# Optimization experiments

Hardware: AMD Instinct MI355X
Metric: run time of the kernel (lower is better)

The kernel has to match this reference:

```python
import jax, jax.numpy as jnp
import numpy as np

TW, NV, EMB, LAYERS = 25, 4, 128, 6
N, E = 65536, 262144
T_MAX = 16.0
EPS = 1e-5

def silu(x):
    return x * jax.nn.sigmoid(x)

def setup_inputs() -> dict:
    key = jax.random.key(0)
    ks = iter(jax.random.split(key, 32))
    def nrm(shape, scale=0.05):
        return jax.random.normal(next(ks), shape, jnp.float32) * scale
    inp = {}
    inp['x'] = jax.random.normal(next(ks), (N, TW), jnp.float32)
    inp['pos'] = jax.random.uniform(next(ks), (N, 1), jnp.float32)
    inp['variables'] = jax.random.uniform(next(ks), (N, NV), jnp.float32)
    inp['dt'] = jnp.full((1,), 0.1, jnp.float32)
    inp['edge_index'] = jax.random.randint(next(ks), (2, E), 0, N)
    inp['enc_W1'] = nrm((TW + NV + 1, EMB)); inp['enc_b1'] = jnp.zeros((EMB,), jnp.float32)
    inp['enc_W2'] = nrm((EMB, EMB));         inp['enc_b2'] = jnp.zeros((EMB,), jnp.float32)
    dmsg = 2 * EMB + TW + 1 + NV   # 286: x_i,x_j,u_i-u_j,pos_i-pos_j,vars_i
    dupd = 2 * EMB + NV            # 260: x, aggregated message, vars
    inp['msg_W1'] = nrm((LAYERS, dmsg, EMB)); inp['msg_b1'] = jnp.zeros((LAYERS, EMB), jnp.float32)
    inp['msg_W2'] = nrm((LAYERS, EMB, EMB));  inp['msg_b2'] = jnp.zeros((LAYERS, EMB), jnp.float32)
    inp['upd_W1'] = nrm((LAYERS, dupd, EMB)); inp['upd_b1'] = jnp.zeros((LAYERS, EMB), jnp.float32)
    inp['upd_W2'] = nrm((LAYERS, EMB, EMB));  inp['upd_b2'] = jnp.zeros((LAYERS, EMB), jnp.float32)
    inp['dec_W1'] = nrm((8, 1, 16)); inp['dec_b1'] = jnp.zeros((8,), jnp.float32)
    inp['dec_W2'] = nrm((1, 8, 14)); inp['dec_b2'] = jnp.zeros((1,), jnp.float32)
    return inp

def reference(x, pos, variables, dt, edge_index,
              enc_W1, enc_b1, enc_W2, enc_b2,
              msg_W1, msg_b1, msg_W2, msg_b2,
              upd_W1, upd_b1, upd_W2, upd_b2,
              dec_W1, dec_b1, dec_W2, dec_b2):
    vars3 = variables[:, :3]              # alpha, beta, gamma
    t = variables[:, 3:4] / T_MAX         # normalized time
    p = pos / jnp.max(pos)                # graph.pos /= pos.max()
    inp0 = jnp.concatenate([x, p, t, vars3], axis=-1)  # [N, 30]
    h = silu(silu(inp0 @ enc_W1 + enc_b1) @ enc_W2 + enc_b2)  # [N, EMB]

    src, dst = edge_index[0], edge_index[1]  # x_j = src, x_i = dst (source_to_target)
    deg = jax.ops.segment_sum(jnp.ones((E,), jnp.float32), dst, num_segments=N)
    inv_deg = (1.0 / jnp.maximum(deg, 1.0))[:, None]

    for l in range(LAYERS):
        m_in = jnp.concatenate(
            [h[dst], h[src], x[dst] - x[src], p[dst] - p[src], variables[dst]], axis=-1)
        m = silu(m_in @ msg_W1[l] + msg_b1[l])
        m = silu(m @ msg_W2[l] + msg_b2[l])                      # [E, EMB]
        agg = jax.ops.segment_sum(m, dst, num_segments=N) * inv_deg  # mean aggr
        u = silu(jnp.concatenate([h, agg, variables], axis=-1) @ upd_W1[l] + upd_b1[l])
        u = silu(u @ upd_W2[l] + upd_b2[l])
        h_new = h + u  # in_features == out_features -> residual
        # PyG InstanceNorm (affine=False), single graph (batch all zeros)
        mu = jnp.mean(h_new, axis=0, keepdims=True)
        var = jnp.var(h_new, axis=0, keepdims=True)
        h = (h_new - mu) * jax.lax.rsqrt(var + EPS)

    # decoder: Conv1d(1->8, k=16, s=3) -> SiLU -> Conv1d(8->1, k=14, s=1)
    z = h[:, None, :]  # [N, 1, EMB]
    z = jax.lax.conv_general_dilated(z, dec_W1, (3,), 'VALID',
                                     dimension_numbers=('NCH', 'OIH', 'NCH')) + dec_b1[None, :, None]
    z = silu(z)
    z = jax.lax.conv_general_dilated(z, dec_W2, (1,), 'VALID',
                                     dimension_numbers=('NCH', 'OIH', 'NCH')) + dec_b2[None, :, None]
    diff = z[:, 0, :]  # [N, TW]
    dtc = dt[0] * jnp.arange(1, TW + 1, dtype=jnp.float32)  # cumsum of dt*ones
    return jnp.tile(x[:, -1:], (1, TW)) + dtc[None, :] * diff
```

## Files before the change

### kernel.cpp

```cpp
#include <hip/hip_runtime.h>
#include <math.h>

#define N_NODES 65536
#define N_EDGES 262144
#define N_LAYERS 6
#define T_MAX_F 16.0f
#define EPS_F 1e-5f

typedef float  f32x4  __attribute__((ext_vector_type(4)));
typedef __bf16 bf16x8 __attribute__((ext_vector_type(8)));

__device__ __forceinline__ float silu_f(float v){
    return v / (1.0f + __expf(-v));
}

__device__ __forceinline__ f32x4 mfma16(bf16x8 a, bf16x8 b, f32x4 c){
    return __builtin_amdgcn_mfma_f32_16x16x32_bf16(a, b, c, 0, 0, 0);
}

#define PK_RA (6 * 20480)
#define PK_RB (6 * 20480)
#define PK_M2 (6 * 16384)
#define PK_U1 (6 * 36864)
#define PK_U2 (6 * 16384)
#define PK_TOTAL (PK_RA + PK_RB + PK_M2 + PK_U1 + PK_U2)

__global__ __launch_bounds__(256) void k_pack(const float* __restrict__ msgW1, const float* __restrict__ msgW2,
                                              const float* __restrict__ updW1, const float* __restrict__ updW2,
                                              __bf16* __restrict__ out){
    int pg = blockIdx.x * 256 + threadIdx.x;
    if (pg >= PK_TOTAL) return;
    int p = pg;
    int mode; const float* W; int perL;
    if (p < PK_RA){ mode = 0; W = msgW1; perL = 20480; }
    else if ((p -= PK_RA) < PK_RB){ mode = 1; W = msgW1; perL = 20480; }
    else if ((p -= PK_RB) < PK_M2){ mode = 2; W = msgW2; perL = 16384; }
    else if ((p -= PK_M2) < PK_U1){ mode = 3; W = updW1; perL = 36864; }
    else { p -= PK_U1; mode = 4; W = updW2; perL = 16384; }
    int l = p / perL, q = p % perL;
    int elem = q & 7, lane = (q >> 3) & 63, cb = (q >> 9) & 7, kb = q >> 12;
    int col = cb * 16 + (lane & 15);
    int k = kb * 32 + ((lane >> 4) << 3) + elem;
    float v = 0.0f;
    if (mode == 0){
        int r = -1;
        if (k < 128) r = k;
        else if (k < 153) r = 256 + (k - 128);
        else if (k == 153) r = 281;
        else if (k < 158) r = 282 + (k - 154);
        if (r >= 0) v = W[(size_t)l * 286 * 128 + (size_t)r * 128 + col];
    } else if (mode == 1){
        if (k < 128) v = W[(size_t)l * 286 * 128 + (size_t)(128 + k) * 128 + col];
        else if (k < 153) v = -W[(size_t)l * 286 * 128 + (size_t)(256 + (k - 128)) * 128 + col];
        else if (k == 153) v = -W[(size_t)l * 286 * 128 + (size_t)281 * 128 + col];
    } else {
        int Kreal = (mode == 3) ? 260 : 128;
        if (k < Kreal) v = W[(size_t)l * Kreal * 128 + (size_t)k * 128 + col];
    }
    out[pg] = (__bf16)v;
}

__global__ __launch_bounds__(256) void k_deg_max(const int* __restrict__ dst, const float* __restrict__ pos,
                                                 int* __restrict__ deg, unsigned* __restrict__ outmax){
    __shared__ float s[256];
    int tid = threadIdx.x;
    int e = blockIdx.x * 256 + tid;
    if (e < N_EDGES) atomicAdd(deg + dst[e], 1);
    if (blockIdx.x < N_NODES / 256){
        s[tid] = pos[blockIdx.x * 256 + tid];
        __syncthreads();
        for (int off = 128; off > 0; off >>= 1){
            if (tid < off) s[tid] = fmaxf(s[tid], s[tid + off]);
            __syncthreads();
        }
        if (tid == 0) atomicMax(outmax, __float_as_uint(s[0]));
    }
}

__global__ __launch_bounds__(256) void k_scan1(const int* __restrict__ deg, int* __restrict__ csum){
    __shared__ int s[256];
    int c = blockIdx.x, t = threadIdx.x;
    s[t] = deg[c * 256 + t];
    __syncthreads();
    for (int o = 128; o > 0; o >>= 1){ if (t < o) s[t] += s[t + o]; __syncthreads(); }
    if (t == 0) csum[c] = s[0];
}

__global__ __launch_bounds__(256) void k_scan2(const int* __restrict__ csum, int* __restrict__ coff){
    __shared__ int s[256];
    int t = threadIdx.x;
    s[t] = csum[t];
    __syncthreads();
    for (int o = 1; o < 256; o <<= 1){
        int v = (t >= o) ? s[t - o] : 0;
        __syncthreads();
        s[t] += v;
        __syncthreads();
    }
    coff[t] = s[t] - csum[t];
}

__global__ __launch_bounds__(256) void k_scan3(const int* __restrict__ deg, const int* __restrict__ coff,
                                               int* __restrict__ cursor){
    __shared__ int s[256];
    int c = blockIdx.x, t = threadIdx.x;
    int d = deg[c * 256 + t];
    s[t] = d;
    __syncthreads();
    for (int o = 1; o < 256; o <<= 1){
        int v = (t >= o) ? s[t - o] : 0;
        __syncthreads();
        s[t] += v;
        __syncthreads();
    }
    cursor[c * 256 + t] = coff[c] + s[t] - d;
}

__global__ __launch_bounds__(256) void k_scatter_prep(const int* __restrict__ esrc, const int* __restrict__ edst,
                                                      int* __restrict__ cursor,
                                                      int* __restrict__ ssrcS, int* __restrict__ sdstS,
                                                      const float* __restrict__ pos, const unsigned* __restrict__ maxp,
                                                      const int* __restrict__ deg,
                                                      float* __restrict__ p, float* __restrict__ invdeg){
    int e = blockIdx.x * 256 + threadIdx.x;
    if (e < N_EDGES){
        int d = edst[e];
        int slot = atomicAdd(cursor + d, 1);
        ssrcS[slot] = esrc[e];
        sdstS[slot] = d;
    }
    if (blockIdx.x < N_NODES / 256){
        int i = blockIdx.x * 256 + threadIdx.x;
        float mp = __uint_as_float(*maxp);
        p[i] = pos[i] / mp;
        invdeg[i] = 1.0f / fmaxf((float)deg[i], 1.0f);
    }
}

__device__ __forceinline__ void gemm44(const float* A, int lda, const float* W,
                                       int kq_begin, int kq_end, int r0, int c0, float acc[4][4]){
    for (int kq = kq_begin; kq < kq_end; ++kq){
        int k = kq * 4;
        float a[4][4], w[4][4];
        #pragma unroll
        for (int i = 0; i < 4; ++i){
            float4 v = *(const float4*)(A + (r0 + i) * lda + k);
            a[i][0] = v.x; a[i][1] = v.y; a[i][2] = v.z; a[i][3] = v.w;
        }
        #pragma unroll
        for (int kk = 0; kk < 4; ++kk){
            float4 v = *(const float4*)(W + (k + kk) * 128 + c0);
            w[kk][0] = v.x; w[kk][1] = v.y; w[kk][2] = v.z; w[kk][3] = v.w;
        }
        #pragma unroll
        for (int kk = 0; kk < 4; ++kk)
            #pragma unroll
            for (int i = 0; i < 4; ++i)
                #pragma unroll
                for (int j = 0; j < 4; ++j)
                    acc[i][j] = fmaf(a[i][kk], w[kk][j], acc[i][j]);
    }
}

__global__ __launch_bounds__(256) void k_enc(const float* __restrict__ x, const float* __restrict__ p,
                                             const float* __restrict__ vars,
                                             const float* __restrict__ W1, const float* __restrict__ b1,
                                             const float* __restrict__ W2, const float* __restrict__ b2,
                                             float* __restrict__ hA){
    __shared__ __align__(16) float sin_[32 * 32];
    __shared__ __align__(16) float swA[32 * 128];
    __shared__ __align__(16) float sy[32 * 128];
    int tid = threadIdx.x;
    int n0 = blockIdx.x * 32;
    for (int i = tid; i < 32 * 32; i += 256){
        int e = i >> 5, k = i & 31;
        int node = n0 + e;
        float v;
        if (k < 25)       v = x[node * 25 + k];
        else if (k == 25) v = p[node];
        else if (k == 26) v = vars[node * 4 + 3] * (1.0f / T_MAX_F);
        else if (k < 30)  v = vars[node * 4 + (k - 27)];
        else              v = 0.0f;
        sin_[e * 32 + k] = v;
    }
    for (int i = tid; i < 32 * 128; i += 256){
        int r = i >> 7;
        swA[i] = (r < 30) ? W1[i] : 0.0f;
    }
    __syncthreads();
    int c0 = (tid & 31) * 4, r0 = (tid >> 5) * 4;
    {
        float acc[4][4] = {};
        gemm44(sin_, 32, swA, 0, 8, r0, c0, acc);
        float4 bv = *(const float4*)(b1 + c0);
        float b_[4] = {bv.x, bv.y, bv.z, bv.w};
        #pragma unroll
        for (int i = 0; i < 4; ++i){
            float4 o;
            o.x = silu_f(acc[i][0] + b_[0]);
            o.y = silu_f(acc[i][1] + b_[1]);
            o.z = silu_f(acc[i][2] + b_[2]);
            o.w = silu_f(acc[i][3] + b_[3]);
            *(float4*)(sy + (r0 + i) * 128 + c0) = o;
        }
    }
    float acc2[4][4] = {};
    for (int c = 0; c < 4; ++c){
        __syncthreads();
        for (int i = tid; i < 1024; i += 256)
            ((float4*)swA)[i] = ((const float4*)(W2 + (size_t)c * 32 * 128))[i];
        __syncthreads();
        gemm44(sy + c * 32, 128, swA, 0, 8, r0, c0, acc2);
    }
    float4 b2v = *(const float4*)(b2 + c0);
    float bb[4] = {b2v.x, b2v.y, b2v.z, b2v.w};
    #pragma unroll
    for (int i = 0; i < 4; ++i){
        float4 o;
        o.x = silu_f(acc2[i][0] + bb[0]);
        o.y = silu_f(acc2[i][1] + bb[1]);
        o.z = silu_f(acc2[i][2] + bb[2]);
        o.w = silu_f(acc2[i][3] + bb[3]);
        *(float4*)(hA + (size_t)(n0 + r0 + i) * 128 + c0) = o;
    }
}

__global__ __launch_bounds__(256) void k_npre(const float* __restrict__ hA, const float* __restrict__ x,
                                              const float* __restrict__ p, const float* __restrict__ vars,
                                              const float* __restrict__ statPrev, int apply_ln,
                                              const __bf16* __restrict__ Wra, const __bf16* __restrict__ Wrb,
                                              const float* __restrict__ b1,
                                              __bf16* __restrict__ raO, __bf16* __restrict__ rbO,
                                              float* __restrict__ aggZ, float* __restrict__ statCurZ){
    __shared__ __align__(16) __bf16 sA[10 * 64 * 8];
    __shared__ __align__(16) float sOut[32 * 264];
    __shared__ __align__(16) float smu[128], sistd[128];
    int tid = threadIdx.x;
    int n0 = blockIdx.x * 32;
    if (apply_ln && tid < 128){
        float m = statPrev[tid] * (1.0f / N_NODES);
        float v = statPrev[128 + tid] * (1.0f / N_NODES) - m * m;
        smu[tid] = m;
        sistd[tid] = rsqrtf(v + EPS_F);
    }
    if (blockIdx.x == 0) statCurZ[tid] = 0.f;
    {
        float4 z4 = {0.f, 0.f, 0.f, 0.f};
        #pragma unroll
        for (int it = 0; it < 4; ++it){
            int i = tid + it * 256;
            int e = i >> 5, ch = i & 31;
            *(float4*)(aggZ + (size_t)(n0 + e) * 128 + ch * 4) = z4;
        }
    }
    __syncthreads();
    #pragma unroll
    for (int it = 0; it < 3; ++it){
        int j = tid + it * 256;
        if (j < 640){
            int f = j >> 6, lane = j & 63;
            int kb = f >> 1, mt = f & 1;
            int e = (lane & 15) + mt * 16, kh = lane >> 4;
            int node = n0 + e;
            bf16x8 o;
            if (kb < 4){
                int k0 = kb * 32 + kh * 8;
                float4 v0 = *(const float4*)(hA + (size_t)node * 128 + k0);
                float4 v1 = *(const float4*)(hA + (size_t)node * 128 + k0 + 4);
                if (apply_ln){
                    float4 m0 = *(const float4*)(smu + k0),   m1 = *(const float4*)(smu + k0 + 4);
                    float4 s0 = *(const float4*)(sistd + k0), s1 = *(const float4*)(sistd + k0 + 4);
                    v0.x = (v0.x - m0.x) * s0.x; v0.y = (v0.y - m0.y) * s0.y;
                    v0.z = (v0.z - m0.z) * s0.z; v0.w = (v0.w - m0.w) * s0.w;
                    v1.x = (v1.x - m1.x) * s1.x; v1.y = (v1.y - m1.y) * s1.y;
                    v1.z = (v1.z - m1.z) * s1.z; v1.w = (v1.w - m1.w) * s1.w;
                }
                o[0] = (__bf16)v0.x; o[1] = (__bf16)v0.y; o[2] = (__bf16)v0.z; o[3] = (__bf16)v0.w;
                o[4] = (__bf16)v1.x; o[5] = (__bf16)v1.y; o[6] = (__bf16)v1.z; o[7] = (__bf16)v1.w;
            } else {
                #pragma unroll
                for (int jj = 0; jj < 8; ++jj){
                    int fk = kh * 8 + jj;
                    float v;
                    if (fk < 25)       v = x[node * 25 + fk];
                    else if (fk == 25) v = p[node];
                    else if (fk < 30)  v = vars[node * 4 + (fk - 26)];
                    else               v = 0.0f;
                    o[jj] = (__bf16)v;
                }
            }
            *(bf16x8*)(sA + (f * 64 + lane) * 8) = o;
        }
    }
    __syncthreads();
    int w = tid >> 6, lane = tid & 63;
    int clo = lane & 15, rhi = lane >> 4;
    f32x4 z = {0.f, 0.f, 0.f, 0.f};
    f32x4 aR[2][2] = {{z, z}, {z, z}};
    f32x4 aB[2][2] = {{z, z}, {z, z}};
    #pragma unroll
    for (int kb = 0; kb < 5; ++kb){
        bf16x8 a0 = *(bf16x8*)(sA + ((kb * 2 + 0) * 64 + lane) * 8);
        bf16x8 a1 = *(bf16x8*)(sA + ((kb * 2 + 1) * 64 + lane) * 8);
        bf16x8 wr0 = *(const bf16x8*)(Wra + (size_t)((kb * 8 + 2 * w)     * 64 + lane) * 8);
        bf16x8 wr1 = *(const bf16x8*)(Wra + (size_t)((kb * 8 + 2 * w + 1) * 64 + lane) * 8);
        bf16x8 wb0 = *(const bf16x8*)(Wrb + (size_t)((kb * 8 + 2 * w)     * 64 + lane) * 8);
        bf16x8 wb1 = *(const bf16x8*)(Wrb + (size_t)((kb * 8 + 2 * w + 1) * 64 + lane) * 8);
        aR[0][0] = mfma16(a0, wr0, aR[0][0]);
        aR[0][1] = mfma16(a0, wr1, aR[0][1]);
        aR[1][0] = mfma16(a1, wr0, aR[1][0]);
        aR[1][1] = mfma16(a1, wr1, aR[1][1]);
        aB[0][0] = mfma16(a0, wb0, aB[0][0]);
        aB[0][1] = mfma16(a0, wb1, aB[0][1]);
        aB[1][0] = mfma16(a1, wb0, aB[1][0]);
        aB[1][1] = mfma16(a1, wb1, aB[1][1]);
    }
    #pragma unroll
    for (int nf = 0; nf < 2; ++nf){
        int col = (2 * w + nf) * 16 + clo;
        float bv = b1[col];
        #pragma unroll
        for (int mt = 0; mt < 2; ++mt)
            #pragma unroll
            for (int i = 0; i < 4; ++i){
                int e = mt * 16 + rhi * 4 + i;
                sOut[e * 264 + col]       = aR[mt][nf][i] + bv;
                sOut[e * 264 + 128 + col] = aB[mt][nf][i];
            }
    }
    __syncthreads();
    #pragma unroll
    for (int it = 0; it < 4; ++it){
        int j = tid + it * 256;
        int row = j >> 5, c8 = j & 31;
        const float* src = sOut + row * 264 + c8 * 8;
        bf16x8 o;
        #pragma unroll
        for (int t = 0; t < 8; ++t) o[t] = (__bf16)src[t];
        __bf16* dstp = (c8 < 16) ? (raO + (size_t)(n0 + row) * 128 + c8 * 8)
                                 : (rbO + (size_t)(n0 + row) * 128 + (c8 - 16) * 8);
        *(bf16x8*)dstp = o;
    }
}

__global__ __launch_bounds__(256) void k_edge3(const __bf16* __restrict__ ra, const __bf16* __restrict__ rb,
                                               const int* __restrict__ ssrcS, const int* __restrict__ sdstS,
                                               const __bf16* __restrict__ Wp2, const float* __restrict__ bias2,
                                               float* __restrict__ agg){
    __shared__ __align__(16) unsigned char smem[64 * 128 * 4];
    __shared__ int sd[64], ss[64];
    __bf16* sA   = (__bf16*)smem;
    float*  msum = (float*)smem;
    int tid = threadIdx.x;
    int e0 = blockIdx.x * 64;
    if (tid < 64){ sd[tid] = sdstS[e0 + tid]; ss[tid] = ssrcS[e0 + tid]; }
    __syncthreads();
    #pragma unroll
    for (int it = 0; it < 4; ++it){
        int j = tid + it * 256;
        int f = j >> 6, lane = j & 63;
        int kb = f >> 2, mt = f & 3;
        int e = (lane & 15) + mt * 16;
        int k0 = kb * 32 + (lane >> 4) * 8;
        bf16x8 va = *(const bf16x8*)(ra + (size_t)sd[e] * 128 + k0);
        bf16x8 vb = *(const bf16x8*)(rb + (size_t)ss[e] * 128 + k0);
        bf16x8 o;
        #pragma unroll
        for (int t = 0; t < 8; ++t)
            o[t] = (__bf16)silu_f((float)va[t] + (float)vb[t]);
        *(bf16x8*)(sA + (f * 64 + lane) * 8) = o;
    }
    __syncthreads();
    int w = tid >> 6, lane = tid & 63;
    int cb0 = 2 * w, clo = lane & 15, rhi = lane >> 4;
    f32x4 z = {0.f, 0.f, 0.f, 0.f};
    f32x4 acc[4][2] = {{z, z}, {z, z}, {z, z}, {z, z}};
    #pragma unroll
    for (int kb = 0; kb < 4; ++kb){
        bf16x8 a0 = *(bf16x8*)(sA + ((kb * 4 + 0) * 64 + lane) * 8);
        bf16x8 a1 = *(bf16x8*)(sA + ((kb * 4 + 1) * 64 + lane) * 8);
        bf16x8 a2 = *(bf16x8*)(sA + ((kb * 4 + 2) * 64 + lane) * 8);
        bf16x8 a3 = *(bf16x8*)(sA + ((kb * 4 + 3) * 64 + lane) * 8);
        bf16x8 w0 = *(const bf16x8*)(Wp2 + (size_t)((kb * 8 + cb0)     * 64 + lane) * 8);
        bf16x8 w1 = *(const bf16x8*)(Wp2 + (size_t)((kb * 8 + cb0 + 1) * 64 + lane) * 8);
        acc[0][0] = mfma16(a0, w0, acc[0][0]);
        acc[0][1] = mfma16(a0, w1, acc[0][1]);
        acc[1][0] = mfma16(a1, w0, acc[1][0]);
        acc[1][1] = mfma16(a1, w1, acc[1][1]);
        acc[2][0] = mfma16(a2, w0, acc[2][0]);
        acc[2][1] = mfma16(a2, w1, acc[2][1]);
        acc[3][0] = mfma16(a3, w0, acc[3][0]);
        acc[3][1] = mfma16(a3, w1, acc[3][1]);
    }
    __syncthreads();
    #pragma unroll
    for (int nf = 0; nf < 2; ++nf){
        int col = (cb0 + nf) * 16 + clo;
        float bv = bias2[col];
        #pragma unroll
        for (int mt = 0; mt < 4; ++mt)
            #pragma unroll
            for (int i = 0; i < 4; ++i){
                int row = mt * 16 + rhi * 4 + i;
                msum[row * 128 + col] = silu_f(acc[mt][nf][i] + bv);
            }
    }
    __syncthreads();
    int col = tid & 127, half = tid >> 7;
    int base = half * 32;
    float run = 0.0f;
    for (int r = 0; r < 32; ++r){
        int row = base + r;
        run += msum[row * 128 + col];
        bool flush = (r == 31) || (sd[row + 1] != sd[row]);
        if (flush){
            atomicAdd(agg + (size_t)sd[row] * 128 + col, run);
            run = 0.0f;
        }
    }
}

__global__ __launch_bounds__(256) void k_upd_m(float* __restrict__ hA, const float* __restrict__ agg,
                                               const float* __restrict__ vars, const float* __restrict__ invdeg,
                                               const float* __restrict__ statPrev, int apply_ln,
                                               const __bf16* __restrict__ Wp1, const float* __restrict__ bias1,
                                               const __bf16* __restrict__ Wp2, const float* __restrict__ bias2,
                                               float* __restrict__ statCur){
    __shared__ __align__(16) __bf16 sA1[36 * 64 * 8];
    __shared__ __align__(16) float smu[128], sistd[128];
    __bf16* zb = sA1;
    int tid = threadIdx.x;
    int n0 = blockIdx.x * 64;
    if (apply_ln && tid < 128){
        float m = statPrev[tid] * (1.0f / N_NODES);
        float v = statPrev[128 + tid] * (1.0f / N_NODES) - m * m;
        smu[tid] = m;
        sistd[tid] = rsqrtf(v + EPS_F);
    }
    __syncthreads();
    #pragma unroll
    for (int it = 0; it < 9; ++it){
        int idx = tid + it * 256;
        int f = idx >> 6, lane = idx & 63;
        int kb = f >> 2, mt = f & 3;
        int row = (lane & 15) + mt * 16;
        int node = n0 + row;
        int k0 = kb * 32 + ((lane >> 4) << 3);
        bf16x8 o;
        if (k0 < 128){
            float4 v0 = *(const float4*)(hA + (size_t)node * 128 + k0);
            float4 v1 = *(const float4*)(hA + (size_t)node * 128 + k0 + 4);
            if (apply_ln){
                float4 m0 = *(const float4*)(smu + k0),   m1 = *(const float4*)(smu + k0 + 4);
                float4 s0 = *(const float4*)(sistd + k0), s1 = *(const float4*)(sistd + k0 + 4);
                v0.x = (v0.x - m0.x) * s0.x; v0.y = (v0.y - m0.y) * s0.y;
                v0.z = (v0.z - m0.z) * s0.z; v0.w = (v0.w - m0.w) * s0.w;
                v1.x = (v1.x - m1.x) * s1.x; v1.y = (v1.y - m1.y) * s1.y;
                v1.z = (v1.z - m1.z) * s1.z; v1.w = (v1.w - m1.w) * s1.w;
            }
            o[0] = (__bf16)v0.x; o[1] = (__bf16)v0.y; o[2] = (__bf16)v0.z; o[3] = (__bf16)v0.w;
            o[4] = (__bf16)v1.x; o[5] = (__bf16)v1.y; o[6] = (__bf16)v1.z; o[7] = (__bf16)v1.w;
        } else if (k0 < 256){
            int g0 = k0 - 128;
            float4 v0 = *(const float4*)(agg + (size_t)node * 128 + g0);
            float4 v1 = *(const float4*)(agg + (size_t)node * 128 + g0 + 4);
            float s = invdeg[node];
            o[0] = (__bf16)(v0.x * s); o[1] = (__bf16)(v0.y * s); o[2] = (__bf16)(v0.z * s); o[3] = (__bf16)(v0.w * s);
            o[4] = (__bf16)(v1.x * s); o[5] = (__bf16)(v1.y * s); o[6] = (__bf16)(v1.z * s); o[7] = (__bf16)(v1.w * s);
        } else {
            int fk = k0 - 256;
            #pragma unroll
            for (int jj = 0; jj < 8; ++jj){
                int kk = fk + jj;
                o[jj] = (__bf16)((kk < 4) ? vars[(size_t)node * 4 + kk] : 0.0f);
            }
        }
        *(bf16x8*)(sA1 + (size_t)idx * 8) = o;
    }
    __syncthreads();
    int w = tid >> 6, lane = tid & 63;
    int cb0 = 2 * w, clo = lane & 15, rhi = lane >> 4;
    f32x4 z = {0.f, 0.f, 0.f, 0.f};
    f32x4 acc[4][2] = {{z, z}, {z, z}, {z, z}, {z, z}};
    #pragma unroll
    for (int kb = 0; kb < 9; ++kb){
        bf16x8 w0 = *(const bf16x8*)(Wp1 + (size_t)((kb * 8 + cb0)     * 64 + lane) * 8);
        bf16x8 w1 = *(const bf16x8*)(Wp1 + (size_t)((kb * 8 + cb0 + 1) * 64 + lane) * 8);
        #pragma unroll
        for (int mt = 0; mt < 4; ++mt){
            bf16x8 a = *(bf16x8*)(sA1 + ((kb * 4 + mt) * 64 + lane) * 8);
            acc[mt][0] = mfma16(a, w0, acc[mt][0]);
            acc[mt][1] = mfma16(a, w1, acc[mt][1]);
        }
    }
    __syncthreads();
    #pragma unroll
    for (int nf = 0; nf < 2; ++nf){
        int col = (cb0 + nf) * 16 + clo;
        float bv = bias1[col];
        #pragma unroll
        for (int mt = 0; mt < 4; ++mt)
            #pragma unroll
            for (int i = 0; i < 4; ++i){
                int row = mt * 16 + rhi * 4 + i;
                zb[row * 152 + col] = (__bf16)silu_f(acc[mt][nf][i] + bv);
            }
    }
    __syncthreads();
    f32x4 acc2[4][2] = {{z, z}, {z, z}, {z, z}, {z, z}};
    #pragma unroll
    for (int kb = 0; kb < 4; ++kb){
        bf16x8 w0 = *(const bf16x8*)(Wp2 + (size_t)((kb * 8 + cb0)     * 64 + lane) * 8);
        bf16x8 w1 = *(const bf16x8*)(Wp2 + (size_t)((kb * 8 + cb0 + 1) * 64 + lane) * 8);
        int k0 = kb * 32 + ((lane >> 4) << 3);
        #pragma unroll
        for (int mt = 0; mt < 4; ++mt){
            int row = (lane & 15) + mt * 16;
            bf16x8 a = *(bf16x8*)(zb + row * 152 + k0);
            acc2[mt][0] = mfma16(a, w0, acc2[mt][0]);
            acc2[mt][1] = mfma16(a, w1, acc2[mt][1]);
        }
    }
    float sm[2] = {0.f, 0.f}, sq[2] = {0.f, 0.f};
    #pragma unroll
    for (int nf = 0; nf < 2; ++nf){
        int col = (cb0 + nf) * 16 + clo;
        float bv = bias2[col];
        float muv = apply_ln ? smu[col] : 0.0f;
        float sdv = apply_ln ? sistd[col] : 1.0f;
        #pragma unroll
        for (int mt = 0; mt < 4; ++mt)
            #pragma unroll
            for (int i = 0; i < 4; ++i){
                int row = mt * 16 + rhi * 4 + i;
                size_t idx = (size_t)(n0 + row) * 128 + col;
                float u = silu_f(acc2[mt][nf][i] + bv);
                float hln = (hA[idx] - muv) * sdv;
                float hv = hln + u;
                hA[idx] = hv;
                sm[nf] += hv; sq[nf] += hv * hv;
            }
    }
    #pragma unroll
    for (int nf = 0; nf < 2; ++nf){
        float s = sm[nf], q = sq[nf];
        s += __shfl_xor(s, 16); q += __shfl_xor(q, 16);
        s += __shfl_xor(s, 32); q += __shfl_xor(q, 32);
        if (rhi == 0){
            int col = (cb0 + nf) * 16 + clo;
            atomicAdd(statCur + col, s);
            atomicAdd(statCur + 128 + col, q);
        }
    }
}

#define DECNB 16
__global__ __launch_bounds__(256) void k_dec(const float* __restrict__ h, const float* __restrict__ x,
                                             const float* __restrict__ dt,
                                             const float* __restrict__ W1, const float* __restrict__ b1,
                                             const float* __restrict__ W2, const float* __restrict__ b2,
                                             const float* __restrict__ statPrev,
                                             float* __restrict__ out){
    __shared__ __align__(16) float sh[DECNB * 132];
    __shared__ __align__(16) float so[DECNB * 312];
    __shared__ float pp[DECNB * 8 * 26];
    __shared__ float sw1[128], sw2[112], sb1[8];
    __shared__ __align__(16) float smu[128], sistd[128];
    int tid = threadIdx.x;
    int n0 = blockIdx.x * DECNB;
    if (tid < 128){
        float m = statPrev[tid] * (1.0f / N_NODES);
        float v = statPrev[128 + tid] * (1.0f / N_NODES) - m * m;
        smu[tid] = m;
        sistd[tid] = rsqrtf(v + EPS_F);
        sw1[tid] = W1[tid];
    } else if (tid < 240) sw2[tid - 128] = W2[tid - 128];
    if (tid < 8) sb1[tid] = b1[tid];
    __syncthreads();
    for (int i = tid; i < DECNB * 32; i += 256){
        int g = i >> 5, chunk = i & 31;
        float4 v = *(const float4*)(h + (size_t)(n0 + g) * 128 + chunk * 4);
        float4 m = *(const float4*)(smu + chunk * 4);
        float4 s = *(const float4*)(sistd + chunk * 4);
        v.x = (v.x - m.x) * s.x; v.y = (v.y - m.y) * s.y;
        v.z = (v.z - m.z) * s.z; v.w = (v.w - m.w) * s.w;
        *(float4*)(sh + g * 132 + chunk * 4) = v;
    }
    __syncthreads();
    {
        int g = tid >> 4, c = (tid >> 1) & 7, jh = tid & 1;
        int j0 = jh * 19;
        float w[16];
        #pragma unroll
        for (int k = 0; k < 16; ++k) w[k] = sw1[c * 16 + k];
        float bc = sb1[c];
        float win[16];
        #pragma unroll
        for (int k = 0; k < 16; ++k) win[k] = sh[g * 132 + 3 * j0 + k];
        #pragma unroll
        for (int j = 0; j < 19; ++j){
            float a = bc;
            #pragma unroll
            for (int k = 0; k < 16; ++k) a = fmaf(win[k], w[k], a);
            so[g * 312 + c * 38 + j0 + j] = silu_f(a);
            if (j < 18){
                #pragma unroll
                for (int k = 0; k < 13; ++k) win[k] = win[k + 3];
                int base = g * 132 + 3 * (j0 + j + 1) + 13;
                win[13] = sh[base]; win[14] = sh[base + 1]; win[15] = sh[base + 2];
            }
        }
    }
    __syncthreads();
    {
        int g = tid >> 4, c = (tid >> 1) & 7, th = tid & 1;
        int t0 = th * 13;
        int nt = th ? 12 : 13;
        float w[14];
        #pragma unroll
        for (int k = 0; k < 14; ++k) w[k] = sw2[c * 14 + k];
        float win[14];
        #pragma unroll
        for (int k = 0; k < 14; ++k) win[k] = so[g * 312 + c * 38 + t0 + k];
        #pragma unroll
        for (int t = 0; t < 13; ++t){
            if (t < nt){
                float a = 0.0f;
                #pragma unroll
                for (int k = 0; k < 14; ++k) a = fmaf(win[k], w[k], a);
                pp[(g * 8 + c) * 26 + t0 + t] = a;
            }
            if (t + 1 < nt){
                #pragma unroll
                for (int k = 0; k < 13; ++k) win[k] = win[k + 1];
                win[13] = so[g * 312 + c * 38 + t0 + t + 14];
            }
        }
    }
    __syncthreads();
    float dtv = dt[0];
    for (int i = tid; i < DECNB * 25; i += 256){
        int g = i / 25, t = i % 25;
        float a = b2[0];
        #pragma unroll
        for (int c = 0; c < 8; ++c) a += pp[(g * 8 + c) * 26 + t];
        out[(size_t)(n0 + g) * 25 + t] = x[(size_t)(n0 + g) * 25 + 24] + dtv * (float)(t + 1) * a;
    }
}

extern "C" void kernel_launch(void* const* d_in, const int* in_sizes, int n_in,
                              void* d_out, int out_size, void* d_ws, size_t ws_size,
                              hipStream_t stream){
    (void)in_sizes; (void)n_in; (void)out_size; (void)ws_size;
    const float* x      = (const float*)d_in[0];
    const float* pos    = (const float*)d_in[1];
    const float* vars   = (const float*)d_in[2];
    const float* dt     = (const float*)d_in[3];
    const int*   ei     = (const int*)d_in[4];
    const float* encW1  = (const float*)d_in[5];
    const float* encb1  = (const float*)d_in[6];
    const float* encW2  = (const float*)d_in[7];
    const float* encb2  = (const float*)d_in[8];
    const float* msgW1  = (const float*)d_in[9];
    const float* msgb1  = (const float*)d_in[10];
    const float* msgW2  = (const float*)d_in[11];
    const float* msgb2  = (const float*)d_in[12];
    const float* updW1  = (const float*)d_in[13];
    const float* updb1  = (const float*)d_in[14];
    const float* updW2  = (const float*)d_in[15];
    const float* updb2  = (const float*)d_in[16];
    const float* decW1  = (const float*)d_in[17];
    const float* decb1  = (const float*)d_in[18];
    const float* decW2  = (const float*)d_in[19];
    const float* decb2  = (const float*)d_in[20];
    float* out = (float*)d_out;

    float* ws = (float*)d_ws;
    size_t off = 0;
    float* hA      = ws + off; off += (size_t)N_NODES * 128;
    float* agg     = ws + off; off += (size_t)N_NODES * 128;
    float* sstat   = ws + off; off += 2 * 256;
    float* p       = ws + off; off += N_NODES;
    float* invdeg  = ws + off; off += N_NODES;
    int* deg       = (int*)(ws + off); off += N_NODES;
    unsigned* maxp = (unsigned*)(ws + off); off += 2;
    int* csum      = (int*)(ws + off); off += 256;
    int* coff      = (int*)(ws + off); off += 256;
    int* cursor    = (int*)(ws + off); off += N_NODES;
    int* ssrcS     = (int*)(ws + off); off += N_EDGES;
    int* sdstS     = (int*)(ws + off); off += N_EDGES;
    __bf16* wpack  = (__bf16*)(ws + off); off += (PK_TOTAL + 1) / 2;
    __bf16* raB    = (__bf16*)(ws + off); off += (size_t)N_NODES * 64;
    __bf16* rbB    = (__bf16*)(ws + off); off += (size_t)N_NODES * 64;

    __bf16* pra = wpack;
    __bf16* prb = pra + PK_RA;
    __bf16* pm2 = prb + PK_RB;
    __bf16* pu1 = pm2 + PK_M2;
    __bf16* pu2 = pu1 + PK_U1;

    const int* esrc = ei;
    const int* edst = ei + N_EDGES;

    hipMemsetAsync(deg, 0, (size_t)N_NODES * sizeof(int) + sizeof(unsigned), stream);

    k_pack<<<(PK_TOTAL + 255) / 256, 256, 0, stream>>>(msgW1, msgW2, updW1, updW2, wpack);
    k_deg_max<<<N_EDGES / 256, 256, 0, stream>>>(edst, pos, deg, maxp);
    k_scan1<<<256, 256, 0, stream>>>(deg, csum);
    k_scan2<<<1, 256, 0, stream>>>(csum, coff);
    k_scan3<<<256, 256, 0, stream>>>(deg, coff, cursor);
    k_scatter_prep<<<N_EDGES / 256, 256, 0, stream>>>(esrc, edst, cursor, ssrcS, sdstS,
                                                      pos, maxp, deg, p, invdeg);
    k_enc<<<N_NODES / 32, 256, 0, stream>>>(x, p, vars, encW1, encb1, encW2, encb2, hA);

    for (int l = 0; l < N_LAYERS; ++l){
        int cur = l & 1;
        float* statCur        = sstat + (size_t)cur * 256;
        const float* statPrev = sstat + (size_t)(cur ^ 1) * 256;
        k_npre<<<N_NODES / 32, 256, 0, stream>>>(hA, x, p, vars, statPrev, (l > 0) ? 1 : 0,
            pra + (size_t)l * 20480, prb + (size_t)l * 20480, msgb1 + l * 128,
            raB, rbB, agg, statCur);
        k_edge3<<<N_EDGES / 64, 256, 0, stream>>>(raB, rbB, ssrcS, sdstS,
            pm2 + (size_t)l * 16384, msgb2 + l * 128, agg);
        k_upd_m<<<N_NODES / 64, 256, 0, stream>>>(hA, agg, vars, invdeg, statPrev, (l > 0) ? 1 : 0,
            pu1 + (size_t)l * 36864, updb1 + l * 128,
            pu2 + (size_t)l * 16384, updb2 + l * 128, statCur);
    }

    k_dec<<<N_NODES / DECNB, 256, 0, stream>>>(hA, x, dt, decW1, decb1, decW2, decb2,
                                               sstat + 256, out);
}
```

Baseline: 880.3 us.

## Shrink shared memory footprints across encoder, node, edge and update kernels

```diff
diff --git a/kernel.cpp b/kernel.cpp
--- a/kernel.cpp
+++ b/kernel.cpp
@@ -168,7 +168,7 @@
                                              const float* __restrict__ W2, const float* __restrict__ b2,
                                              float* __restrict__ hA){
     __shared__ __align__(16) float sin_[32 * 32];
-    __shared__ __align__(16) float swA[32 * 128];
+    __shared__ __align__(16) float swA[24 * 128];
     __shared__ __align__(16) float sy[32 * 128];
     int tid = threadIdx.x;
     int n0 = blockIdx.x * 32;
@@ -183,15 +183,22 @@
         else              v = 0.0f;
         sin_[e * 32 + k] = v;
     }
-    for (int i = tid; i < 32 * 128; i += 256){
-        int r = i >> 7;
-        swA[i] = (r < 30) ? W1[i] : 0.0f;
-    }
-    __syncthreads();
     int c0 = (tid & 31) * 4, r0 = (tid >> 5) * 4;
+    float acc[4][4] = {};
+    #pragma unroll
+    for (int c = 0; c < 2; ++c){
+        int cs = c * 24, nr = c ? 8 : 24;
+        __syncthreads();
+        for (int i = tid; i < nr * 32; i += 256){
+            int gr = cs + (i >> 5);
+            float4 v = {0.f, 0.f, 0.f, 0.f};
+            if (gr < 30) v = *(const float4*)(W1 + gr * 128 + (i & 31) * 4);
+            ((float4*)swA)[i] = v;
+        }
+        __syncthreads();
+        gemm44(sin_ + cs, 32, swA, 0, nr >> 2, r0, c0, acc);
+    }
     {
-        float acc[4][4] = {};
-        gemm44(sin_, 32, swA, 0, 8, r0, c0, acc);
         float4 bv = *(const float4*)(b1 + c0);
         float b_[4] = {bv.x, bv.y, bv.z, bv.w};
         #pragma unroll
@@ -205,12 +212,13 @@
         }
     }
     float acc2[4][4] = {};
-    for (int c = 0; c < 4; ++c){
-        __syncthreads();
-        for (int i = tid; i < 1024; i += 256)
-            ((float4*)swA)[i] = ((const float4*)(W2 + (size_t)c * 32 * 128))[i];
-        __syncthreads();
-        gemm44(sy + c * 32, 128, swA, 0, 8, r0, c0, acc2);
+    for (int c = 0; c < 6; ++c){
+        int cs = c * 24, nr = (c < 5) ? 24 : 8;
+        __syncthreads();
+        for (int i = tid; i < nr * 32; i += 256)
+            ((float4*)swA)[i] = *(const float4*)(W2 + (size_t)(cs + (i >> 5)) * 128 + (i & 31) * 4);
+        __syncthreads();
+        gemm44(sy + cs, 128, swA, 0, nr >> 2, r0, c0, acc2);
     }
     float4 b2v = *(const float4*)(b2 + c0);
     float bb[4] = {b2v.x, b2v.y, b2v.z, b2v.w};
@@ -233,7 +241,7 @@
                                               __bf16* __restrict__ raO, __bf16* __restrict__ rbO,
                                               float* __restrict__ aggZ, float* __restrict__ statCurZ){
     __shared__ __align__(16) __bf16 sA[10 * 64 * 8];
-    __shared__ __align__(16) float sOut[32 * 264];
+    __shared__ __align__(16) __bf16 sOutB[32 * 264];
     __shared__ __align__(16) float smu[128], sistd[128];
     int tid = threadIdx.x;
     int n0 = blockIdx.x * 32;
@@ -324,8 +332,8 @@
             #pragma unroll
             for (int i = 0; i < 4; ++i){
                 int e = mt * 16 + rhi * 4 + i;
-                sOut[e * 264 + col]       = aR[mt][nf][i] + bv;
-                sOut[e * 264 + 128 + col] = aB[mt][nf][i];
+                sOutB[e * 264 + col]       = (__bf16)(aR[mt][nf][i] + bv);
+                sOutB[e * 264 + 128 + col] = (__bf16)aB[mt][nf][i];
             }
     }
     __syncthreads();
@@ -333,10 +341,7 @@
     for (int it = 0; it < 4; ++it){
         int j = tid + it * 256;
         int row = j >> 5, c8 = j & 31;
-        const float* src = sOut + row * 264 + c8 * 8;
-        bf16x8 o;
-        #pragma unroll
-        for (int t = 0; t < 8; ++t) o[t] = (__bf16)src[t];
+        bf16x8 o = *(bf16x8*)(sOutB + row * 264 + c8 * 8);
         __bf16* dstp = (c8 < 16) ? (raO + (size_t)(n0 + row) * 128 + c8 * 8)
                                  : (rbO + (size_t)(n0 + row) * 128 + (c8 - 16) * 8);
         *(bf16x8*)dstp = o;
@@ -347,10 +352,9 @@
                                                const int* __restrict__ ssrcS, const int* __restrict__ sdstS,
                                                const __bf16* __restrict__ Wp2, const float* __restrict__ bias2,
                                                float* __restrict__ agg){
-    __shared__ __align__(16) unsigned char smem[64 * 128 * 4];
+    __shared__ __align__(16) __bf16 sA[16 * 64 * 8];
     __shared__ int sd[64], ss[64];
-    __bf16* sA   = (__bf16*)smem;
-    float*  msum = (float*)smem;
+    float* msum32 = (float*)sA;
     int tid = threadIdx.x;
     int e0 = blockIdx.x * 64;
     if (tid < 64){ sd[tid] = sdstS[e0 + tid]; ss[tid] = ssrcS[e0 + tid]; }
@@ -394,29 +398,38 @@
     }
     __syncthreads();
     #pragma unroll
-    for (int nf = 0; nf < 2; ++nf){
-        int col = (cb0 + nf) * 16 + clo;
-        float bv = bias2[col];
-        #pragma unroll
-        for (int mt = 0; mt < 4; ++mt)
+    for (int pass = 0; pass < 2; ++pass){
+        #pragma unroll
+        for (int nf = 0; nf < 2; ++nf){
+            int col = (cb0 + nf) * 16 + clo;
+            float bv = bias2[col];
             #pragma unroll
-            for (int i = 0; i < 4; ++i){
-                int row = mt * 16 + rhi * 4 + i;
-                msum[row * 128 + col] = silu_f(acc[mt][nf][i] + bv);
-            }
-    }
-    __syncthreads();
-    int col = tid & 127, half = tid >> 7;
-    int base = half * 32;
-    float run = 0.0f;
-    for (int r = 0; r < 32; ++r){
-        int row = base + r;
-        run += msum[row * 128 + col];
-        bool flush = (r == 31) || (sd[row + 1] != sd[row]);
-        if (flush){
-            atomicAdd(agg + (size_t)sd[row] * 128 + col, run);
-            run = 0.0f;
-        }
+            for (int ml = 0; ml < 2; ++ml){
+                int mt = pass * 2 + ml;
+                #pragma unroll
+                for (int i = 0; i < 4; ++i){
+                    int lr = ml * 16 + rhi * 4 + i;
+                    msum32[lr * 128 + col] = silu_f(acc[mt][nf][i] + bv);
+                }
+            }
+        }
+        __syncthreads();
+        {
+            int col = tid & 127, h = tid >> 7;
+            int lbase = h * 16;
+            float run = 0.0f;
+            for (int r = 0; r < 16; ++r){
+                int lr = lbase + r;
+                int grow = pass * 32 + lr;
+                run += msum32[lr * 128 + col];
+                bool flush = (r == 15) || (sd[grow + 1] != sd[grow]);
+                if (flush){
+                    atomicAdd(agg + (size_t)sd[grow] * 128 + col, run);
+                    run = 0.0f;
+                }
+            }
+        }
+        __syncthreads();
     }
 }
 
@@ -426,11 +439,11 @@
                                                const __bf16* __restrict__ Wp1, const float* __restrict__ bias1,
                                                const __bf16* __restrict__ Wp2, const float* __restrict__ bias2,
                                                float* __restrict__ statCur){
-    __shared__ __align__(16) __bf16 sA1[36 * 64 * 8];
+    __shared__ __align__(16) __bf16 sA1[18 * 64 * 8];
     __shared__ __align__(16) float smu[128], sistd[128];
     __bf16* zb = sA1;
     int tid = threadIdx.x;
-    int n0 = blockIdx.x * 64;
+    int n0 = blockIdx.x * 32;
     if (apply_ln && tid < 128){
         float m = statPrev[tid] * (1.0f / N_NODES);
         float v = statPrev[128 + tid] * (1.0f / N_NODES) - m * m;
@@ -439,56 +452,58 @@
     }
     __syncthreads();
     #pragma unroll
-    for (int it = 0; it < 9; ++it){
+    for (int it = 0; it < 5; ++it){
         int idx = tid + it * 256;
-        int f = idx >> 6, lane = idx & 63;
-        int kb = f >> 2, mt = f & 3;
-        int row = (lane & 15) + mt * 16;
-        int node = n0 + row;
-        int k0 = kb * 32 + ((lane >> 4) << 3);
-        bf16x8 o;
-        if (k0 < 128){
-            float4 v0 = *(const float4*)(hA + (size_t)node * 128 + k0);
-            float4 v1 = *(const float4*)(hA + (size_t)node * 128 + k0 + 4);
-            if (apply_ln){
-                float4 m0 = *(const float4*)(smu + k0),   m1 = *(const float4*)(smu + k0 + 4);
-                float4 s0 = *(const float4*)(sistd + k0), s1 = *(const float4*)(sistd + k0 + 4);
-                v0.x = (v0.x - m0.x) * s0.x; v0.y = (v0.y - m0.y) * s0.y;
-                v0.z = (v0.z - m0.z) * s0.z; v0.w = (v0.w - m0.w) * s0.w;
-                v1.x = (v1.x - m1.x) * s1.x; v1.y = (v1.y - m1.y) * s1.y;
-                v1.z = (v1.z - m1.z) * s1.z; v1.w = (v1.w - m1.w) * s1.w;
-            }
-            o[0] = (__bf16)v0.x; o[1] = (__bf16)v0.y; o[2] = (__bf16)v0.z; o[3] = (__bf16)v0.w;
-            o[4] = (__bf16)v1.x; o[5] = (__bf16)v1.y; o[6] = (__bf16)v1.z; o[7] = (__bf16)v1.w;
-        } else if (k0 < 256){
-            int g0 = k0 - 128;
-            float4 v0 = *(const float4*)(agg + (size_t)node * 128 + g0);
-            float4 v1 = *(const float4*)(agg + (size_t)node * 128 + g0 + 4);
-            float s = invdeg[node];
-            o[0] = (__bf16)(v0.x * s); o[1] = (__bf16)(v0.y * s); o[2] = (__bf16)(v0.z * s); o[3] = (__bf16)(v0.w * s);
-            o[4] = (__bf16)(v1.x * s); o[5] = (__bf16)(v1.y * s); o[6] = (__bf16)(v1.z * s); o[7] = (__bf16)(v1.w * s);
-        } else {
-            int fk = k0 - 256;
-            #pragma unroll
-            for (int jj = 0; jj < 8; ++jj){
-                int kk = fk + jj;
-                o[jj] = (__bf16)((kk < 4) ? vars[(size_t)node * 4 + kk] : 0.0f);
-            }
-        }
-        *(bf16x8*)(sA1 + (size_t)idx * 8) = o;
+        if (idx < 1152){
+            int f = idx >> 6, lane = idx & 63;
+            int kb = f >> 1, mt = f & 1;
+            int row = (lane & 15) + mt * 16;
+            int node = n0 + row;
+            int k0 = kb * 32 + ((lane >> 4) << 3);
+            bf16x8 o;
+            if (k0 < 128){
+                float4 v0 = *(const float4*)(hA + (size_t)node * 128 + k0);
+                float4 v1 = *(const float4*)(hA + (size_t)node * 128 + k0 + 4);
+                if (apply_ln){
+                    float4 m0 = *(const float4*)(smu + k0),   m1 = *(const float4*)(smu + k0 + 4);
+                    float4 s0 = *(const float4*)(sistd + k0), s1 = *(const float4*)(sistd + k0 + 4);
+                    v0.x = (v0.x - m0.x) * s0.x; v0.y = (v0.y - m0.y) * s0.y;
+                    v0.z = (v0.z - m0.z) * s0.z; v0.w = (v0.w - m0.w) * s0.w;
+                    v1.x = (v1.x - m1.x) * s1.x; v1.y = (v1.y - m1.y) * s1.y;
+                    v1.z = (v1.z - m1.z) * s1.z; v1.w = (v1.w - m1.w) * s1.w;
+                }
+                o[0] = (__bf16)v0.x; o[1] = (__bf16)v0.y; o[2] = (__bf16)v0.z; o[3] = (__bf16)v0.w;
+                o[4] = (__bf16)v1.x; o[5] = (__bf16)v1.y; o[6] = (__bf16)v1.z; o[7] = (__bf16)v1.w;
+            } else if (k0 < 256){
+                int g0 = k0 - 128;
+                float4 v0 = *(const float4*)(agg + (size_t)node * 128 + g0);
+                float4 v1 = *(const float4*)(agg + (size_t)node * 128 + g0 + 4);
+                float s = invdeg[node];
+                o[0] = (__bf16)(v0.x * s); o[1] = (__bf16)(v0.y * s); o[2] = (__bf16)(v0.z * s); o[3] = (__bf16)(v0.w * s);
+                o[4] = (__bf16)(v1.x * s); o[5] = (__bf16)(v1.y * s); o[6] = (__bf16)(v1.z * s); o[7] = (__bf16)(v1.w * s);
+            } else {
+                int fk = k0 - 256;
+                #pragma unroll
+                for (int jj = 0; jj < 8; ++jj){
+                    int kk = fk + jj;
+                    o[jj] = (__bf16)((kk < 4) ? vars[(size_t)node * 4 + kk] : 0.0f);
+                }
+            }
+            *(bf16x8*)(sA1 + (size_t)idx * 8) = o;
+        }
     }
     __syncthreads();
     int w = tid >> 6, lane = tid & 63;
     int cb0 = 2 * w, clo = lane & 15, rhi = lane >> 4;
     f32x4 z = {0.f, 0.f, 0.f, 0.f};
-    f32x4 acc[4][2] = {{z, z}, {z, z}, {z, z}, {z, z}};
+    f32x4 acc[2][2] = {{z, z}, {z, z}};
     #pragma unroll
     for (int kb = 0; kb < 9; ++kb){
         bf16x8 w0 = *(const bf16x8*)(Wp1 + (size_t)((kb * 8 + cb0)     * 64 + lane) * 8);
         bf16x8 w1 = *(const bf16x8*)(Wp1 + (size_t)((kb * 8 + cb0 + 1) * 64 + lane) * 8);
         #pragma unroll
-        for (int mt = 0; mt < 4; ++mt){
-            bf16x8 a = *(bf16x8*)(sA1 + ((kb * 4 + mt) * 64 + lane) * 8);
+        for (int mt = 0; mt < 2; ++mt){
+            bf16x8 a = *(bf16x8*)(sA1 + ((kb * 2 + mt) * 64 + lane) * 8);
             acc[mt][0] = mfma16(a, w0, acc[mt][0]);
             acc[mt][1] = mfma16(a, w1, acc[mt][1]);
         }
@@ -499,7 +514,7 @@
         int col = (cb0 + nf) * 16 + clo;
         float bv = bias1[col];
         #pragma unroll
-        for (int mt = 0; mt < 4; ++mt)
+        for (int mt = 0; mt < 2; ++mt)
             #pragma unroll
             for (int i = 0; i < 4; ++i){
                 int row = mt * 16 + rhi * 4 + i;
@@ -507,14 +522,14 @@
             }
     }
     __syncthreads();
-    f32x4 acc2[4][2] = {{z, z}, {z, z}, {z, z}, {z, z}};
+    f32x4 acc2[2][2] = {{z, z}, {z, z}};
     #pragma unroll
     for (int kb = 0; kb < 4; ++kb){
         bf16x8 w0 = *(const bf16x8*)(Wp2 + (size_t)((kb * 8 + cb0)     * 64 + lane) * 8);
         bf16x8 w1 = *(const bf16x8*)(Wp2 + (size_t)((kb * 8 + cb0 + 1) * 64 + lane) * 8);
         int k0 = kb * 32 + ((lane >> 4) << 3);
         #pragma unroll
-        for (int mt = 0; mt < 4; ++mt){
+        for (int mt = 0; mt < 2; ++mt){
             int row = (lane & 15) + mt * 16;
             bf16x8 a = *(bf16x8*)(zb + row * 152 + k0);
             acc2[mt][0] = mfma16(a, w0, acc2[mt][0]);
@@ -529,7 +544,7 @@
         float muv = apply_ln ? smu[col] : 0.0f;
         float sdv = apply_ln ? sistd[col] : 1.0f;
         #pragma unroll
-        for (int mt = 0; mt < 4; ++mt)
+        for (int mt = 0; mt < 2; ++mt)
             #pragma unroll
             for (int i = 0; i < 4; ++i){
                 int row = mt * 16 + rhi * 4 + i;
@@ -722,7 +737,7 @@
             raB, rbB, agg, statCur);
         k_edge3<<<N_EDGES / 64, 256, 0, stream>>>(raB, rbB, ssrcS, sdstS,
             pm2 + (size_t)l * 16384, msgb2 + l * 128, agg);
-        k_upd_m<<<N_NODES / 64, 256, 0, stream>>>(hA, agg, vars, invdeg, statPrev, (l > 0) ? 1 : 0,
+        k_upd_m<<<N_NODES / 32, 256, 0, stream>>>(hA, agg, vars, invdeg, statPrev, (l > 0) ? 1 : 0,
             pu1 + (size_t)l * 36864, updb1 + l * 128,
             pu2 + (size_t)l * 16384, updb2 + l * 128, statCur);
     }
```

New measurement: 2.133 ms. 142% more time.
